# Kernel tuning notes

Hardware: AMD Instinct MI355X
Metric: run time of the kernel (lower is better)

## Reference

```python
import jax, jax.numpy as jnp
import numpy as np

N = 50000
E = 800000
IN_DIM, HID, HEADS, OUT_DIM = 32, 64, 4, 128
HC = HID * HEADS  # 256
LN_EPS = 1e-5
NEG_SLOPE = 0.2


def setup_inputs() -> dict:
    key = jax.random.key(0)
    ks = jax.random.split(key, 16)
    s = 0.05
    inp = {
        "x": jax.random.normal(ks[0], (N, IN_DIM), dtype=jnp.float32),
        "edge_index": jax.random.randint(ks[1], (2, E), 0, N, dtype=jnp.int32),
        # input projection
        "W_in": jax.random.normal(ks[2], (IN_DIM, HID), dtype=jnp.float32) * s,
        "b_in": jnp.zeros((HID,), dtype=jnp.float32),
        # GAT layer 0: in=HID, out=HID per head, HEADS heads
        "lin0_w": jax.random.normal(ks[3], (HID, HC), dtype=jnp.float32) * s,
        "att0_src": jax.random.normal(ks[4], (HEADS, HID), dtype=jnp.float32) * s,
        "att0_dst": jax.random.normal(ks[5], (HEADS, HID), dtype=jnp.float32) * s,
        "bias0": jnp.zeros((HC,), dtype=jnp.float32),
        # GAT layer 1: in=HC, out=HID per head
        "lin1_w": jax.random.normal(ks[6], (HC, HC), dtype=jnp.float32) * s,
        "att1_src": jax.random.normal(ks[7], (HEADS, HID), dtype=jnp.float32) * s,
        "att1_dst": jax.random.normal(ks[8], (HEADS, HID), dtype=jnp.float32) * s,
        "bias1": jnp.zeros((HC,), dtype=jnp.float32),
        # output projection + layernorm
        "W_out": jax.random.normal(ks[9], (HC, OUT_DIM), dtype=jnp.float32) * s,
        "b_out": jnp.zeros((OUT_DIM,), dtype=jnp.float32),
        "ln_gamma": jnp.ones((OUT_DIM,), dtype=jnp.float32),
        "ln_beta": jnp.zeros((OUT_DIM,), dtype=jnp.float32),
    }
    return inp


def _gat_conv(x, src, dst, lin_w, att_src, att_dst, bias):
    # x: [N, F_in]; src/dst: [E'] (self-loops included)
    h = (x @ lin_w).reshape(N, HEADS, HID)           # [N, H, C]
    a_src = jnp.einsum("nhc,hc->nh", h, att_src)      # [N, H]
    a_dst = jnp.einsum("nhc,hc->nh", h, att_dst)      # [N, H]
    e = a_src[src] + a_dst[dst]                        # [E', H]
    e = jnp.where(e > 0, e, NEG_SLOPE * e)             # leaky_relu(0.2)
    # segment softmax over incoming edges per destination
    m = jax.ops.segment_max(e, dst, num_segments=N)    # [N, H]
    p = jnp.exp(e - m[dst])
    denom = jax.ops.segment_sum(p, dst, num_segments=N)
    alpha = p / (denom[dst] + 1e-16)                   # [E', H]
    msg = h[src] * alpha[:, :, None]                   # [E', H, C]
    out = jax.ops.segment_sum(msg, dst, num_segments=N)  # [N, H, C]
    return out.reshape(N, HC) + bias


def reference(x, edge_index, W_in, b_in, lin0_w, att0_src, att0_dst, bias0,
              lin1_w, att1_src, att1_dst, bias1, W_out, b_out, ln_gamma, ln_beta):
    # add self-loops (PyG GATConv default)
    loops = jnp.arange(N, dtype=edge_index.dtype)
    src = jnp.concatenate([edge_index[0], loops])
    dst = jnp.concatenate([edge_index[1], loops])

    h = jax.nn.elu(x @ W_in + b_in)
    h = jax.nn.elu(_gat_conv(h, src, dst, lin0_w, att0_src, att0_dst, bias0))
    h = jax.nn.elu(_gat_conv(h, src, dst, lin1_w, att1_src, att1_dst, bias1))
    h = h @ W_out + b_out
    mu = jnp.mean(h, axis=-1, keepdims=True)
    var = jnp.mean((h - mu) ** 2, axis=-1, keepdims=True)
    return (h - mu) * jax.lax.rsqrt(var + LN_EPS) * ln_gamma + ln_beta
```

## Files before the change

kernel.cpp:

```cpp
#include <hip/hip_runtime.h>
#include <cstdint>

#define N_NODES 50000
#define N_EDGES 800000
#define EP (N_EDGES + N_NODES)
#define IN_DIM 32
#define HID 64
#define HEADS 4
#define HC 256
#define OUT_DIM 128
#define NEG_SLOPE 0.2f
#define LN_EPS 1e-5f
#define SCAN_B 1024
#define NB ((N_NODES + SCAN_B - 1) / SCAN_B)

typedef __attribute__((ext_vector_type(8))) short bf16x8;
typedef __attribute__((ext_vector_type(16))) float f32x16;

__device__ __forceinline__ unsigned bf16rne(float f) {
    unsigned u = __float_as_uint(f);
    return (u + 0x7fffu + ((u >> 16) & 1u)) >> 16;
}
__device__ __forceinline__ unsigned pack_bf2(float a, float b) {
    return bf16rne(a) | (bf16rne(b) << 16);
}
__device__ __forceinline__ float bf_lo(unsigned w) { return __uint_as_float(w << 16); }
__device__ __forceinline__ float bf_hi_raw(unsigned w) { return __uint_as_float(w); }

#define PREP_INPROJ ((N_NODES * HID) / 256)
#define PREP_WPACK ((HID * HC + HC * HC + HC * OUT_DIM) / 256)
#define PREP_EXT 40
#define PREP_HIST ((EP + 255) / 256)
__global__ void k_prep(const float* __restrict__ x, const float* __restrict__ W_in,
                       const float* __restrict__ b_in, unsigned short* __restrict__ h_in,
                       const float* __restrict__ w0, const float* __restrict__ w1,
                       const float* __restrict__ w2, unsigned short* __restrict__ p0,
                       unsigned short* __restrict__ p1, unsigned short* __restrict__ p2,
                       const float* __restrict__ as0, const float* __restrict__ ad0,
                       unsigned short* __restrict__ ext0,
                       const float* __restrict__ as1, const float* __restrict__ ad1,
                       unsigned short* __restrict__ ext1,
                       const int* __restrict__ ei, int* __restrict__ counts,
                       int* __restrict__ rank) {
    if (blockIdx.x < PREP_INPROJ) {
        int g = blockIdx.x * 256 + threadIdx.x;
        int n = g >> 6, j = g & 63;
        const float* xr = x + n * IN_DIM;
        float acc = b_in[j];
#pragma unroll
        for (int k = 0; k < IN_DIM; ++k) acc += xr[k] * W_in[k * HID + j];
        acc = acc > 0.f ? acc : (__expf(acc) - 1.f);
        h_in[g] = (unsigned short)bf16rne(acc);
    } else if (blockIdx.x < PREP_INPROJ + PREP_WPACK) {
        int g = (blockIdx.x - PREP_INPROJ) * 256 + threadIdx.x;
        if (g < HID * HC) {
            int k = g >> 8, n = g & 255;
            p0[(((k >> 3) * HC) + n) * 8 + (k & 7)] = (unsigned short)bf16rne(w0[g]);
        } else if (g < HID * HC + HC * HC) {
            int t = g - HID * HC;
            int k = t >> 8, n = t & 255;
            p1[(((k >> 3) * HC) + n) * 8 + (k & 7)] = (unsigned short)bf16rne(w1[t]);
        } else {
            int t = g - HID * HC - HC * HC;
            int k = t >> 7, n = t & 127;
            p2[(((k >> 3) * OUT_DIM) + n) * 8 + (k & 7)] = (unsigned short)bf16rne(w2[t]);
        }
    } else if (blockIdx.x < PREP_INPROJ + PREP_WPACK + PREP_EXT) {
        int t = (blockIdx.x - PREP_INPROJ - PREP_WPACK) * 256 + threadIdx.x;
        const float* w; const float* as; const float* ad; unsigned short* ext; int e;
        if (t < 2048) { w = w0; as = as0; ad = ad0; ext = ext0; e = t; }
        else if (t < 2048 + 8192) { w = w1; as = as1; ad = ad1; ext = ext1; e = t - 2048; }
        else return;
        int kb = e >> 8, rem = e & 255, col = rem >> 3, kk = rem & 7;
        int k = kb * 8 + kk;
        float acc = 0.f;
        if (col < 8) {
            int h = col & 3;
            const float* att = (col < 4) ? as : ad;
#pragma unroll 4
            for (int c = 0; c < HID; ++c) acc += w[k * HC + h * HID + c] * att[h * HID + c];
        }
        ext[e] = (unsigned short)bf16rne(acc);
    } else {
        int e = (blockIdx.x - PREP_INPROJ - PREP_WPACK - PREP_EXT) * 256 + threadIdx.x;
        if (e >= EP) return;
        int d = (e < N_EDGES) ? ei[N_EDGES + e] : (e - N_EDGES);
        rank[e] = atomicAdd(&counts[d], 1);
    }
}

__global__ void k_scan(const int* __restrict__ counts, int* __restrict__ bsum,
                       int* __restrict__ done, int* __restrict__ row_ptr) {
    __shared__ int buf[SCAN_B];
    __shared__ int sbase;
    int i = blockIdx.x * SCAN_B + threadIdx.x;
    int v = (i < N_NODES) ? counts[i] : 0;
    buf[threadIdx.x] = v;
    __syncthreads();
    for (int off = 1; off < SCAN_B; off <<= 1) {
        int t = (threadIdx.x >= off) ? buf[threadIdx.x - off] : 0;
        __syncthreads();
        buf[threadIdx.x] += t;
        __syncthreads();
    }
    int excl = buf[threadIdx.x] - v;
    if (threadIdx.x == SCAN_B - 1) {
        bsum[blockIdx.x] = buf[SCAN_B - 1];
        __threadfence();
        atomicAdd(done, 1);
    }
    if (threadIdx.x == 0) {
        while (__hip_atomic_load(done, __ATOMIC_RELAXED, __HIP_MEMORY_SCOPE_AGENT) < NB) {
            __builtin_amdgcn_s_sleep(8);
        }
    }
    __syncthreads();
    if (threadIdx.x < 64) {
        int t = threadIdx.x;
        int val = (t < blockIdx.x)
                ? __hip_atomic_load(&bsum[t], __ATOMIC_RELAXED, __HIP_MEMORY_SCOPE_AGENT) : 0;
#pragma unroll
        for (int mk = 1; mk < 64; mk <<= 1) val += __shfl_xor(val, mk, 64);
        if (t == 0) sbase = val;
    }
    __syncthreads();
    if (i < N_NODES) row_ptr[i] = excl + sbase;
    if (i == 0) row_ptr[N_NODES] = EP;
}

template <int K>
__device__ __forceinline__ void gemm_lin_body(
        int mblk, const unsigned short* __restrict__ A, const unsigned short* __restrict__ Bp,
        const unsigned short* __restrict__ Ext, unsigned short* __restrict__ hh,
        float* __restrict__ a_src, float* __restrict__ a_dst) {
    const int lane = threadIdx.x & 63;
    const int quad = lane >> 5, c = lane & 31;
    const int wave = threadIdx.x >> 6;
    const int m0 = mblk * 64 + (wave >> 1) * 32;
    const int cb = (wave & 1) * 128;
    f32x16 acc[4];
#pragma unroll
    for (int nt = 0; nt < 4; ++nt)
#pragma unroll
        for (int i = 0; i < 16; ++i) acc[nt][i] = 0.f;
    f32x16 acce;
#pragma unroll
    for (int i = 0; i < 16; ++i) acce[i] = 0.f;
    int mrow = m0 + c; if (mrow >= N_NODES) mrow = N_NODES - 1;
    const size_t abase = (size_t)mrow * K + quad * 8;
    for (int k0 = 0; k0 < K; k0 += 16) {
        bf16x8 af = *(const bf16x8*)(A + abase + k0);
        const unsigned short* bk = Bp + ((size_t)(k0 >> 3) + quad) * (HC * 8);
#pragma unroll
        for (int nt = 0; nt < 4; ++nt) {
            bf16x8 bf = *(const bf16x8*)(bk + (cb + nt * 32 + c) * 8);
            acc[nt] = __builtin_amdgcn_mfma_f32_32x32x16_bf16(af, bf, acc[nt], 0, 0, 0);
        }
        if (wave & 1) {
            bf16x8 bfe = *(const bf16x8*)(Ext + ((k0 >> 3) + quad) * 256 + c * 8);
            acce = __builtin_amdgcn_mfma_f32_32x32x16_bf16(af, bfe, acce, 0, 0, 0);
        }
    }
#pragma unroll
    for (int reg = 0; reg < 16; ++reg) {
        int row = (reg & 3) + 8 * (reg >> 2) + 4 * quad;
        int m = m0 + row;
        if (m < N_NODES) {
            size_t base = (size_t)m * HC + cb + c;
#pragma unroll
            for (int nt = 0; nt < 4; ++nt)
                hh[base + nt * 32] = (unsigned short)bf16rne(acc[nt][reg]);
            if ((wave & 1) && c < 8) {
                float v = acce[reg];
                if (c < 4) a_src[m * HEADS + c] = v;
                else       a_dst[m * HEADS + (c - 4)] = v;
            }
        }
    }
}

template <int K>
__global__ __launch_bounds__(256) void k_gemm_lin(
        const unsigned short* __restrict__ A, const unsigned short* __restrict__ Bp,
        const unsigned short* __restrict__ Ext, unsigned short* __restrict__ hh,
        float* __restrict__ a_src, float* __restrict__ a_dst) {
    gemm_lin_body<K>(blockIdx.x, A, Bp, Ext, hh, a_src, a_dst);
}

#define G0_BLOCKS ((N_NODES + 63) / 64)
__global__ __launch_bounds__(256) void k_gemm0_scatter(
        const unsigned short* __restrict__ A, const unsigned short* __restrict__ Bp,
        const unsigned short* __restrict__ Ext, unsigned short* __restrict__ hh,
        float* __restrict__ a_src, float* __restrict__ a_dst,
        const int* __restrict__ ei, const int* __restrict__ row_ptr,
        const int* __restrict__ rank, int* __restrict__ esrc) {
    if (blockIdx.x < G0_BLOCKS) {
        gemm_lin_body<HID>(blockIdx.x, A, Bp, Ext, hh, a_src, a_dst);
        return;
    }
    int e = (blockIdx.x - G0_BLOCKS) * 256 + threadIdx.x;
    if (e < EP) {
        int s, d;
        if (e < N_EDGES) { s = ei[e]; d = ei[N_EDGES + e]; } else { s = d = e - N_EDGES; }
        esrc[row_ptr[d] + rank[e]] = s;
    } else if (e - EP < 64) {
        esrc[e] = 0;
    }
}

__global__ __launch_bounds__(256) void k_gat_agg(
        const int* __restrict__ row_ptr, const int* __restrict__ esrc,
        const unsigned short* __restrict__ hh, const float* __restrict__ a_src,
        const float* __restrict__ a_dst, const float* __restrict__ bias,
        unsigned short* __restrict__ out) {
    const int wave = threadIdx.x >> 6;
    const int lane = threadIdx.x & 63;
    const int half = lane >> 5;
    const int l = lane & 31;
    const int d = blockIdx.x * 8 + wave * 2 + half;
    const int h = l >> 3;
    const unsigned c0 = (unsigned)(l * 8);
    const int bsrc = half << 5;
    const float ad = a_dst[((unsigned)d << 2) + h];
    const int beg = row_ptr[d], end = row_ptr[d + 1];
    float acc[8];
#pragma unroll
    for (int t = 0; t < 8; ++t) acc[t] = 0.f;
    float psum = 0.f;
    int myv = esrc[beg + l];
    for (int base = beg; base < end; base += 32) {
        int rem = end - base;
        int cnt = rem > 32 ? 32 : rem;
        int nxt = 0;
        if (rem > 32) nxt = esrc[base + 32 + l];
        int i = 0;
        for (; i + 4 <= cnt; i += 4) {
            int s0 = __shfl(myv, bsrc + i, 64);
            int s1 = __shfl(myv, bsrc + i + 1, 64);
            int s2 = __shfl(myv, bsrc + i + 2, 64);
            int s3 = __shfl(myv, bsrc + i + 3, 64);
            float as0 = a_src[((unsigned)s0 << 2) + h];
            float as1 = a_src[((unsigned)s1 << 2) + h];
            float as2 = a_src[((unsigned)s2 << 2) + h];
            float as3 = a_src[((unsigned)s3 << 2) + h];
            uint4 g0 = *(const uint4*)(hh + (((unsigned)s0 << 8) + c0));
            uint4 g1 = *(const uint4*)(hh + (((unsigned)s1 << 8) + c0));
            uint4 g2 = *(const uint4*)(hh + (((unsigned)s2 << 8) + c0));
            uint4 g3 = *(const uint4*)(hh + (((unsigned)s3 << 8) + c0));
            float e0 = as0 + ad, e1 = as1 + ad, e2 = as2 + ad, e3 = as3 + ad;
            e0 = fmaxf(e0, NEG_SLOPE * e0); e1 = fmaxf(e1, NEG_SLOPE * e1);
            e2 = fmaxf(e2, NEG_SLOPE * e2); e3 = fmaxf(e3, NEG_SLOPE * e3);
            float p0 = __expf(e0), p1 = __expf(e1), p2 = __expf(e2), p3 = __expf(e3);
            psum += (p0 + p1) + (p2 + p3);
            acc[0] += p0 * bf_lo(g0.x) + p1 * bf_lo(g1.x) + p2 * bf_lo(g2.x) + p3 * bf_lo(g3.x);
            acc[1] += p0 * bf_hi_raw(g0.x) + p1 * bf_hi_raw(g1.x) + p2 * bf_hi_raw(g2.x) + p3 * bf_hi_raw(g3.x);
            acc[2] += p0 * bf_lo(g0.y) + p1 * bf_lo(g1.y) + p2 * bf_lo(g2.y) + p3 * bf_lo(g3.y);
            acc[3] += p0 * bf_hi_raw(g0.y) + p1 * bf_hi_raw(g1.y) + p2 * bf_hi_raw(g2.y) + p3 * bf_hi_raw(g3.y);
            acc[4] += p0 * bf_lo(g0.z) + p1 * bf_lo(g1.z) + p2 * bf_lo(g2.z) + p3 * bf_lo(g3.z);
            acc[5] += p0 * bf_hi_raw(g0.z) + p1 * bf_hi_raw(g1.z) + p2 * bf_hi_raw(g2.z) + p3 * bf_hi_raw(g3.z);
            acc[6] += p0 * bf_lo(g0.w) + p1 * bf_lo(g1.w) + p2 * bf_lo(g2.w) + p3 * bf_lo(g3.w);
            acc[7] += p0 * bf_hi_raw(g0.w) + p1 * bf_hi_raw(g1.w) + p2 * bf_hi_raw(g2.w) + p3 * bf_hi_raw(g3.w);
        }
        for (; i < cnt; ++i) {
            int s0 = __shfl(myv, bsrc + i, 64);
            float as0 = a_src[((unsigned)s0 << 2) + h];
            uint4 g0 = *(const uint4*)(hh + (((unsigned)s0 << 8) + c0));
            float e0 = as0 + ad;
            e0 = fmaxf(e0, NEG_SLOPE * e0);
            float p0 = __expf(e0);
            psum += p0;
            acc[0] += p0 * bf_lo(g0.x); acc[1] += p0 * bf_hi_raw(g0.x);
            acc[2] += p0 * bf_lo(g0.y); acc[3] += p0 * bf_hi_raw(g0.y);
            acc[4] += p0 * bf_lo(g0.z); acc[5] += p0 * bf_hi_raw(g0.z);
            acc[6] += p0 * bf_lo(g0.w); acc[7] += p0 * bf_hi_raw(g0.w);
        }
        myv = nxt;
    }
    const float inv = 1.f / (psum + 1e-16f);
    const float4 bb0 = *(const float4*)(bias + c0);
    const float4 bb1 = *(const float4*)(bias + c0 + 4);
    float v[8];
    v[0] = acc[0] * inv + bb0.x; v[1] = acc[1] * inv + bb0.y;
    v[2] = acc[2] * inv + bb0.z; v[3] = acc[3] * inv + bb0.w;
    v[4] = acc[4] * inv + bb1.x; v[5] = acc[5] * inv + bb1.y;
    v[6] = acc[6] * inv + bb1.z; v[7] = acc[7] * inv + bb1.w;
#pragma unroll
    for (int t = 0; t < 8; ++t) v[t] = v[t] > 0.f ? v[t] : (__expf(v[t]) - 1.f);
    uint4 pk;
    pk.x = pack_bf2(v[0], v[1]); pk.y = pack_bf2(v[2], v[3]);
    pk.z = pack_bf2(v[4], v[5]); pk.w = pack_bf2(v[6], v[7]);
    *(uint4*)(out + (((size_t)d << 8) + c0)) = pk;
}

__global__ __launch_bounds__(256) void k_gemm_out(
        const unsigned short* __restrict__ A, const unsigned short* __restrict__ Bp,
        const float* __restrict__ b, const float* __restrict__ gamma,
        const float* __restrict__ beta, float* __restrict__ out) {
    const int lane = threadIdx.x & 63;
    const int quad = lane >> 5, c = lane & 31;
    const int m0 = blockIdx.x * 128 + (threadIdx.x >> 6) * 32;
    f32x16 acc[4];
#pragma unroll
    for (int nt = 0; nt < 4; ++nt)
#pragma unroll
        for (int i = 0; i < 16; ++i) acc[nt][i] = 0.f;
    int mrow = m0 + c; if (mrow >= N_NODES) mrow = N_NODES - 1;
    const size_t abase = (size_t)mrow * HC + quad * 8;
    for (int k0 = 0; k0 < HC; k0 += 16) {
        bf16x8 af = *(const bf16x8*)(A + abase + k0);
        const unsigned short* bk = Bp + ((size_t)(k0 >> 3) + quad) * (OUT_DIM * 8);
#pragma unroll
        for (int nt = 0; nt < 4; ++nt) {
            bf16x8 bf = *(const bf16x8*)(bk + (nt * 32 + c) * 8);
            acc[nt] = __builtin_amdgcn_mfma_f32_32x32x16_bf16(af, bf, acc[nt], 0, 0, 0);
        }
    }
    float bb[4], gg[4], be[4];
#pragma unroll
    for (int nt = 0; nt < 4; ++nt) {
        int col = nt * 32 + c;
        bb[nt] = b[col]; gg[nt] = gamma[col]; be[nt] = beta[col];
    }
#pragma unroll
    for (int reg = 0; reg < 16; ++reg) {
        int row = (reg & 3) + 8 * (reg >> 2) + 4 * quad;
        int m = m0 + row;
        float v[4];
        float s = 0.f, s2 = 0.f;
#pragma unroll
        for (int nt = 0; nt < 4; ++nt) {
            v[nt] = acc[nt][reg] + bb[nt];
            s += v[nt]; s2 += v[nt] * v[nt];
        }
#pragma unroll
        for (int mk = 1; mk < 32; mk <<= 1) {
            s += __shfl_xor(s, mk, 64);
            s2 += __shfl_xor(s2, mk, 64);
        }
        float mu = s * (1.f / OUT_DIM);
        float var = s2 * (1.f / OUT_DIM) - mu * mu;
        float inv = rsqrtf(var + LN_EPS);
        if (m < N_NODES) {
            size_t base = (size_t)m * OUT_DIM + c;
#pragma unroll
            for (int nt = 0; nt < 4; ++nt)
                out[base + nt * 32] = (v[nt] - mu) * inv * gg[nt] + be[nt];
        }
    }
}

extern "C" void kernel_launch(void* const* d_in, const int* in_sizes, int n_in,
                              void* d_out, int out_size, void* d_ws, size_t ws_size,
                              hipStream_t stream) {
    const float* x        = (const float*)d_in[0];
    const int*   ei       = (const int*)  d_in[1];
    const float* W_in     = (const float*)d_in[2];
    const float* b_in     = (const float*)d_in[3];
    const float* lin0_w   = (const float*)d_in[4];
    const float* att0_src = (const float*)d_in[5];
    const float* att0_dst = (const float*)d_in[6];
    const float* bias0    = (const float*)d_in[7];
    const float* lin1_w   = (const float*)d_in[8];
    const float* att1_src = (const float*)d_in[9];
    const float* att1_dst = (const float*)d_in[10];
    const float* bias1    = (const float*)d_in[11];
    const float* W_out    = (const float*)d_in[12];
    const float* b_out    = (const float*)d_in[13];
    const float* ln_gamma = (const float*)d_in[14];
    const float* ln_beta  = (const float*)d_in[15];
    float* out = (float*)d_out;

    unsigned short* us = (unsigned short*)d_ws;
    unsigned short* h_in_bf = us;
    unsigned short* hh_bf   = h_in_bf + (size_t)N_NODES * HID;
    unsigned short* feat_bf = hh_bf + (size_t)N_NODES * HC;
    unsigned short* p0      = feat_bf + (size_t)N_NODES * HC;
    unsigned short* p1      = p0 + HID * HC;
    unsigned short* p2      = p1 + HC * HC;
    unsigned short* ext0    = p2 + HC * OUT_DIM;
    unsigned short* ext1    = ext0 + 2048;
    float* a_src = (float*)(ext1 + 8192);
    float* a_dst = a_src + (size_t)N_NODES * HEADS;
    int* counts  = (int*)(a_dst + (size_t)N_NODES * HEADS);
    int* done    = counts + N_NODES;
    int* bsum    = done + 1;
    int* row_ptr = bsum + NB;
    int* rank    = row_ptr + N_NODES + 1;
    int* esrc    = rank + EP;

    hipMemsetAsync(counts, 0, (N_NODES + 1) * sizeof(int), stream);

    k_prep<<<PREP_INPROJ + PREP_WPACK + PREP_EXT + PREP_HIST, 256, 0, stream>>>(
        x, W_in, b_in, h_in_bf, lin0_w, lin1_w, W_out, p0, p1, p2,
        att0_src, att0_dst, ext0, att1_src, att1_dst, ext1, ei, counts, rank);

    k_scan<<<NB, SCAN_B, 0, stream>>>(counts, bsum, done, row_ptr);

    k_gemm0_scatter<<<G0_BLOCKS + PREP_HIST, 256, 0, stream>>>(
        h_in_bf, p0, ext0, hh_bf, a_src, a_dst, ei, row_ptr, rank, esrc);
    k_gat_agg<<<N_NODES / 8, 256, 0, stream>>>(row_ptr, esrc, hh_bf, a_src, a_dst,
                                               bias0, feat_bf);

    k_gemm_lin<HC><<<(N_NODES + 63) / 64, 256, 0, stream>>>(feat_bf, p1, ext1, hh_bf,
                                                            a_src, a_dst);
    k_gat_agg<<<N_NODES / 8, 256, 0, stream>>>(row_ptr, esrc, hh_bf, a_src, a_dst,
                                               bias1, feat_bf);

    k_gemm_out<<<(N_NODES + 127) / 128, 256, 0, stream>>>(feat_bf, p2, b_out,
                                                          ln_gamma, ln_beta, out);
}
```

Before: 357.7 us.

## Fuse GAT aggregation with following GEMM via per-tile completion counters

Merges each aggregation kernel with the next dense GEMM into one launch. Consumer GEMM blocks spin on per-row-tile atomic counters until the aggregation blocks covering their rows finish. This lets GEMM tiles start while other aggregation work is still running and removes two launch boundaries. Separate hh/a_src buffers per layer are added so consumers never overwrite data that producers are still reading. The scheme relies on consumer blocks being dispatched after their producers to avoid deadlock, and the spinning blocks hold CU slots while they wait.

Result: slower. 801.9 us (+124.2%).

```diff
diff --git a/kernel.cpp b/kernel.cpp
--- a/kernel.cpp
+++ b/kernel.cpp
@@ -13,6 +13,9 @@
 #define LN_EPS 1e-5f
 #define SCAN_B 1024
 #define NB ((N_NODES + SCAN_B - 1) / SCAN_B)
+#define AGG_BLOCKS (N_NODES / 8)
+#define LIN_BLOCKS ((N_NODES + 63) / 64)
+#define OUT_BLOCKS ((N_NODES + 127) / 128)
 
 typedef __attribute__((ext_vector_type(8))) short bf16x8;
 typedef __attribute__((ext_vector_type(16))) float f32x16;
@@ -179,26 +182,17 @@
     }
 }
 
-template <int K>
-__global__ __launch_bounds__(256) void k_gemm_lin(
-        const unsigned short* __restrict__ A, const unsigned short* __restrict__ Bp,
-        const unsigned short* __restrict__ Ext, unsigned short* __restrict__ hh,
-        float* __restrict__ a_src, float* __restrict__ a_dst) {
-    gemm_lin_body<K>(blockIdx.x, A, Bp, Ext, hh, a_src, a_dst);
-}
-
-#define G0_BLOCKS ((N_NODES + 63) / 64)
 __global__ __launch_bounds__(256) void k_gemm0_scatter(
         const unsigned short* __restrict__ A, const unsigned short* __restrict__ Bp,
         const unsigned short* __restrict__ Ext, unsigned short* __restrict__ hh,
         float* __restrict__ a_src, float* __restrict__ a_dst,
         const int* __restrict__ ei, const int* __restrict__ row_ptr,
         const int* __restrict__ rank, int* __restrict__ esrc) {
-    if (blockIdx.x < G0_BLOCKS) {
+    if (blockIdx.x < LIN_BLOCKS) {
         gemm_lin_body<HID>(blockIdx.x, A, Bp, Ext, hh, a_src, a_dst);
         return;
     }
-    int e = (blockIdx.x - G0_BLOCKS) * 256 + threadIdx.x;
+    int e = (blockIdx.x - LIN_BLOCKS) * 256 + threadIdx.x;
     if (e < EP) {
         int s, d;
         if (e < N_EDGES) { s = ei[e]; d = ei[N_EDGES + e]; } else { s = d = e - N_EDGES; }
@@ -208,8 +202,8 @@
     }
 }
 
-__global__ __launch_bounds__(256) void k_gat_agg(
-        const int* __restrict__ row_ptr, const int* __restrict__ esrc,
+__device__ __forceinline__ void agg_body(
+        int blk, const int* __restrict__ row_ptr, const int* __restrict__ esrc,
         const unsigned short* __restrict__ hh, const float* __restrict__ a_src,
         const float* __restrict__ a_dst, const float* __restrict__ bias,
         unsigned short* __restrict__ out) {
@@ -217,7 +211,7 @@
     const int lane = threadIdx.x & 63;
     const int half = lane >> 5;
     const int l = lane & 31;
-    const int d = blockIdx.x * 8 + wave * 2 + half;
+    const int d = blk * 8 + wave * 2 + half;
     const int h = l >> 3;
     const unsigned c0 = (unsigned)(l * 8);
     const int bsrc = half << 5;
@@ -243,10 +237,10 @@
             float as1 = a_src[((unsigned)s1 << 2) + h];
             float as2 = a_src[((unsigned)s2 << 2) + h];
             float as3 = a_src[((unsigned)s3 << 2) + h];
-            uint4 g0 = *(const uint4*)(hh + (((unsigned)s0 << 8) + c0));
-            uint4 g1 = *(const uint4*)(hh + (((unsigned)s1 << 8) + c0));
-            uint4 g2 = *(const uint4*)(hh + (((unsigned)s2 << 8) + c0));
-            uint4 g3 = *(const uint4*)(hh + (((unsigned)s3 << 8) + c0));
+            uint4 g0 = *(const uint4*)(hh + (((size_t)(unsigned)s0 << 8) + c0));
+            uint4 g1 = *(const uint4*)(hh + (((size_t)(unsigned)s1 << 8) + c0));
+            uint4 g2 = *(const uint4*)(hh + (((size_t)(unsigned)s2 << 8) + c0));
+            uint4 g3 = *(const uint4*)(hh + (((size_t)(unsigned)s3 << 8) + c0));
             float e0 = as0 + ad, e1 = as1 + ad, e2 = as2 + ad, e3 = as3 + ad;
             e0 = fmaxf(e0, NEG_SLOPE * e0); e1 = fmaxf(e1, NEG_SLOPE * e1);
             e2 = fmaxf(e2, NEG_SLOPE * e2); e3 = fmaxf(e3, NEG_SLOPE * e3);
@@ -264,7 +258,7 @@
         for (; i < cnt; ++i) {
             int s0 = __shfl(myv, bsrc + i, 64);
             float as0 = a_src[((unsigned)s0 << 2) + h];
-            uint4 g0 = *(const uint4*)(hh + (((unsigned)s0 << 8) + c0));
+            uint4 g0 = *(const uint4*)(hh + (((size_t)(unsigned)s0 << 8) + c0));
             float e0 = as0 + ad;
             e0 = fmaxf(e0, NEG_SLOPE * e0);
             float p0 = __expf(e0);
@@ -292,13 +286,62 @@
     *(uint4*)(out + (((size_t)d << 8) + c0)) = pk;
 }
 
-__global__ __launch_bounds__(256) void k_gemm_out(
-        const unsigned short* __restrict__ A, const unsigned short* __restrict__ Bp,
-        const float* __restrict__ b, const float* __restrict__ gamma,
-        const float* __restrict__ beta, float* __restrict__ out) {
+__global__ __launch_bounds__(256) void k_agg_gemm1(
+        const int* __restrict__ row_ptr, const int* __restrict__ esrc,
+        const unsigned short* __restrict__ hh_a, const float* __restrict__ a_srcA,
+        const float* __restrict__ a_dstA, const float* __restrict__ bias0,
+        unsigned short* __restrict__ feat,
+        const unsigned short* __restrict__ p1, const unsigned short* __restrict__ ext1,
+        unsigned short* __restrict__ hh_b, float* __restrict__ a_srcB,
+        float* __restrict__ a_dstB, int* __restrict__ cnt1) {
+    if (blockIdx.x < AGG_BLOCKS) {
+        agg_body(blockIdx.x, row_ptr, esrc, hh_a, a_srcA, a_dstA, bias0, feat);
+        __syncthreads();
+        if (threadIdx.x == 0) {
+            __threadfence();
+            atomicAdd(&cnt1[blockIdx.x >> 3], 1);
+        }
+        return;
+    }
+    const int g = blockIdx.x - AGG_BLOCKS;
+    const int target = (8 * g + 8 <= AGG_BLOCKS) ? 8 : (AGG_BLOCKS - 8 * g);
+    if (threadIdx.x == 0) {
+        while (__hip_atomic_load(&cnt1[g], __ATOMIC_RELAXED, __HIP_MEMORY_SCOPE_AGENT) < target)
+            __builtin_amdgcn_s_sleep(2);
+        __threadfence();
+    }
+    __syncthreads();
+    gemm_lin_body<HC>(g, feat, p1, ext1, hh_b, a_srcB, a_dstB);
+}
+
+__global__ __launch_bounds__(256) void k_agg_gemm2(
+        const int* __restrict__ row_ptr, const int* __restrict__ esrc,
+        const unsigned short* __restrict__ hh_b, const float* __restrict__ a_srcB,
+        const float* __restrict__ a_dstB, const float* __restrict__ bias1,
+        unsigned short* __restrict__ feat,
+        const unsigned short* __restrict__ p2, const float* __restrict__ b,
+        const float* __restrict__ gamma, const float* __restrict__ beta,
+        float* __restrict__ out, int* __restrict__ cnt2) {
+    if (blockIdx.x < AGG_BLOCKS) {
+        agg_body(blockIdx.x, row_ptr, esrc, hh_b, a_srcB, a_dstB, bias1, feat);
+        __syncthreads();
+        if (threadIdx.x == 0) {
+            __threadfence();
+            atomicAdd(&cnt2[blockIdx.x >> 4], 1);
+        }
+        return;
+    }
+    const int g = blockIdx.x - AGG_BLOCKS;
+    const int target = (16 * g + 16 <= AGG_BLOCKS) ? 16 : (AGG_BLOCKS - 16 * g);
+    if (threadIdx.x == 0) {
+        while (__hip_atomic_load(&cnt2[g], __ATOMIC_RELAXED, __HIP_MEMORY_SCOPE_AGENT) < target)
+            __builtin_amdgcn_s_sleep(2);
+        __threadfence();
+    }
+    __syncthreads();
     const int lane = threadIdx.x & 63;
     const int quad = lane >> 5, c = lane & 31;
-    const int m0 = blockIdx.x * 128 + (threadIdx.x >> 6) * 32;
+    const int m0 = g * 128 + (threadIdx.x >> 6) * 32;
     f32x16 acc[4];
 #pragma unroll
     for (int nt = 0; nt < 4; ++nt)
@@ -307,8 +350,8 @@
     int mrow = m0 + c; if (mrow >= N_NODES) mrow = N_NODES - 1;
     const size_t abase = (size_t)mrow * HC + quad * 8;
     for (int k0 = 0; k0 < HC; k0 += 16) {
-        bf16x8 af = *(const bf16x8*)(A + abase + k0);
-        const unsigned short* bk = Bp + ((size_t)(k0 >> 3) + quad) * (OUT_DIM * 8);
+        bf16x8 af = *(const bf16x8*)(feat + abase + k0);
+        const unsigned short* bk = p2 + ((size_t)(k0 >> 3) + quad) * (OUT_DIM * 8);
 #pragma unroll
         for (int nt = 0; nt < 4; ++nt) {
             bf16x8 bf = *(const bf16x8*)(bk + (nt * 32 + c) * 8);
@@ -372,23 +415,28 @@
 
     unsigned short* us = (unsigned short*)d_ws;
     unsigned short* h_in_bf = us;
-    unsigned short* hh_bf   = h_in_bf + (size_t)N_NODES * HID;
-    unsigned short* feat_bf = hh_bf + (size_t)N_NODES * HC;
+    unsigned short* hh_a    = h_in_bf + (size_t)N_NODES * HID;
+    unsigned short* hh_b    = hh_a + (size_t)N_NODES * HC;
+    unsigned short* feat_bf = hh_b + (size_t)N_NODES * HC;
     unsigned short* p0      = feat_bf + (size_t)N_NODES * HC;
     unsigned short* p1      = p0 + HID * HC;
     unsigned short* p2      = p1 + HC * HC;
     unsigned short* ext0    = p2 + HC * OUT_DIM;
     unsigned short* ext1    = ext0 + 2048;
-    float* a_src = (float*)(ext1 + 8192);
-    float* a_dst = a_src + (size_t)N_NODES * HEADS;
-    int* counts  = (int*)(a_dst + (size_t)N_NODES * HEADS);
+    float* a_srcA = (float*)(ext1 + 8192);
+    float* a_dstA = a_srcA + (size_t)N_NODES * HEADS;
+    float* a_srcB = a_dstA + (size_t)N_NODES * HEADS;
+    float* a_dstB = a_srcB + (size_t)N_NODES * HEADS;
+    int* counts  = (int*)(a_dstB + (size_t)N_NODES * HEADS);
     int* done    = counts + N_NODES;
-    int* bsum    = done + 1;
+    int* cnt1    = done + 1;
+    int* cnt2    = cnt1 + LIN_BLOCKS;
+    int* bsum    = cnt2 + OUT_BLOCKS;
     int* row_ptr = bsum + NB;
     int* rank    = row_ptr + N_NODES + 1;
     int* esrc    = rank + EP;
 
-    hipMemsetAsync(counts, 0, (N_NODES + 1) * sizeof(int), stream);
+    hipMemsetAsync(counts, 0, (N_NODES + 1 + LIN_BLOCKS + OUT_BLOCKS) * sizeof(int), stream);
 
     k_prep<<<PREP_INPROJ + PREP_WPACK + PREP_EXT + PREP_HIST, 256, 0, stream>>>(
         x, W_in, b_in, h_in_bf, lin0_w, lin1_w, W_out, p0, p1, p2,
@@ -396,16 +444,14 @@
 
     k_scan<<<NB, SCAN_B, 0, stream>>>(counts, bsum, done, row_ptr);
 
-    k_gemm0_scatter<<<G0_BLOCKS + PREP_HIST, 256, 0, stream>>>(
-        h_in_bf, p0, ext0, hh_bf, a_src, a_dst, ei, row_ptr, rank, esrc);
-    k_gat_agg<<<N_NODES / 8, 256, 0, stream>>>(row_ptr, esrc, hh_bf, a_src, a_dst,
-                                               bias0, feat_bf);
-
-    k_gemm_lin<HC><<<(N_NODES + 63) / 64, 256, 0, stream>>>(feat_bf, p1, ext1, hh_bf,
-                                                            a_src, a_dst);
-    k_gat_agg<<<N_NODES / 8, 256, 0, stream>>>(row_ptr, esrc, hh_bf, a_src, a_dst,
-                                               bias1, feat_bf);
-
-    k_gemm_out<<<(N_NODES + 127) / 128, 256, 0, stream>>>(feat_bf, p2, b_out,
-                                                          ln_gamma, ln_beta, out);
-}
+    k_gemm0_scatter<<<LIN_BLOCKS + PREP_HIST, 256, 0, stream>>>(
+        h_in_bf, p0, ext0, hh_a, a_srcA, a_dstA, ei, row_ptr, rank, esrc);
+
+    k_agg_gemm1<<<AGG_BLOCKS + LIN_BLOCKS, 256, 0, stream>>>(
+        row_ptr, esrc, hh_a, a_srcA, a_dstA, bias0, feat_bf,
+        p1, ext1, hh_b, a_srcB, a_dstB, cnt1);
+
+    k_agg_gemm2<<<AGG_BLOCKS + OUT_BLOCKS, 256, 0, stream>>>(
+        row_ptr, esrc, hh_b, a_srcB, a_dstB, bias1, feat_bf,
+        p2, b_out, ln_gamma, ln_beta, out, cnt2);
+}
```
